# Kernel optimization log

Hardware: AMD Instinct MI355X
Metric: run time of the kernel (lower is better)

Reference implementation:

```python
import jax, jax.numpy as jnp
import numpy as np

N_NODES = 50000
N_EDGES = 800000
N_GRAPHS = 64
F_IN = 128
HEADS = 4
CH = 32
HID = HEADS * CH  # 128
N_CLASSES = 10
N_LAYERS = 3
NEG_SLOPE = 0.2


def setup_inputs() -> dict:
    key = jax.random.key(0)
    ks = jax.random.split(key, 12)
    x = jax.random.normal(ks[0], (N_NODES, F_IN), dtype=jnp.float32)
    edge_index = jax.random.randint(ks[1], (2, N_EDGES), 0, N_NODES, dtype=jnp.int64)
    batch = jnp.sort(jax.random.randint(ks[2], (N_NODES,), 0, N_GRAPHS, dtype=jnp.int64))
    s = 0.1
    Wl = jax.random.normal(ks[3], (N_LAYERS, F_IN, HID), dtype=jnp.float32) * s
    Wr = jax.random.normal(ks[4], (N_LAYERS, F_IN, HID), dtype=jnp.float32) * s
    bl = jax.random.normal(ks[5], (N_LAYERS, HID), dtype=jnp.float32) * s
    br = jax.random.normal(ks[6], (N_LAYERS, HID), dtype=jnp.float32) * s
    att = jax.random.normal(ks[7], (N_LAYERS, HEADS, CH), dtype=jnp.float32) * s
    bias = jax.random.normal(ks[8], (N_LAYERS, HID), dtype=jnp.float32) * s
    lin_w = jax.random.normal(ks[9], (HID, N_CLASSES), dtype=jnp.float32) * s
    lin_b = jax.random.normal(ks[10], (N_CLASSES,), dtype=jnp.float32) * s
    return {"x": x, "edge_index": edge_index, "batch": batch, "Wl": Wl, "Wr": Wr,
            "bl": bl, "br": br, "att": att, "bias": bias, "lin_w": lin_w, "lin_b": lin_b}


def gatv2_layer(x, Wl, Wr, bl, br, att, bias, src, dst):
    # x: [N, D_in] -> out: [N, HEADS*CH]
    n = x.shape[0]
    xl = (x @ Wl + bl).reshape(n, HEADS, CH)  # source transform
    xr = (x @ Wr + br).reshape(n, HEADS, CH)  # target transform
    # GATv2 edge scores: a^T LeakyReLU(W_l x_j + W_r x_i), per head
    e = jnp.einsum('ehc,hc->eh', jax.nn.leaky_relu(xl[src] + xr[dst], NEG_SLOPE), att)  # [E, H]
    # softmax over edges sharing the same destination node
    m = jax.ops.segment_max(e, dst, num_segments=n)
    ee = jnp.exp(e - m[dst])
    denom = jax.ops.segment_sum(ee, dst, num_segments=n)
    alpha = ee / denom[dst]  # [E, H]
    out = jax.ops.segment_sum(xl[src] * alpha[:, :, None], dst, num_segments=n)  # [N, H, C]
    return out.reshape(n, HID) + bias


def reference(x, edge_index, batch, Wl, Wr, bl, br, att, bias, lin_w, lin_b):
    n = x.shape[0]
    loop = jnp.arange(n, dtype=edge_index.dtype)
    src = jnp.concatenate([edge_index[0], loop])  # self loops (PyG default)
    dst = jnp.concatenate([edge_index[1], loop])
    h = x
    for l in range(N_LAYERS):
        h = jax.nn.elu(gatv2_layer(h, Wl[l], Wr[l], bl[l], br[l], att[l], bias[l], src, dst))
    # global mean pool over graphs
    sums = jax.ops.segment_sum(h, batch, num_segments=N_GRAPHS)
    cnt = jax.ops.segment_sum(jnp.ones((n,), h.dtype), batch, num_segments=N_GRAPHS)
    pooled = sums / jnp.maximum(cnt, 1.0)[:, None]
    logits = jax.nn.elu(pooled @ lin_w + lin_b)
    return jax.nn.log_softmax(logits, axis=1)
```

## Files before the change

### kernel.cpp

```cpp
#include <hip/hip_runtime.h>
#include <hip/hip_bf16.h>
#include <math.h>

#define N_NODES 50000
#define N_EDGES 800000
#define N_GRAPHS 64
#define HID 128
#define N_CLASSES 10
#define N_LAYERS 3
#define NEG_SLOPE 0.2f

#define NB 196
#define BCAP 5120
#define ACHUNK 4096

typedef __attribute__((ext_vector_type(8))) short short8;
typedef __attribute__((ext_vector_type(4))) float f32x4;
typedef __attribute__((ext_vector_type(2))) _Float16 h2;

extern "C" __device__ _Float16 __ocml_exp2_f16(_Float16);

__device__ inline ushort f2bf(float f) {
    uint u = __builtin_bit_cast(uint, f);
    u += 0x7fffu + ((u >> 16) & 1u);
    return (ushort)(u >> 16);
}
__device__ inline uint pk2bf(float a, float b) {
    return (uint)f2bf(a) | ((uint)f2bf(b) << 16);
}
__device__ inline h2 pkh(float a, float b) {
    return __builtin_bit_cast(h2, __builtin_amdgcn_cvt_pkrtz(a, b));
}


__global__ __launch_bounds__(256) void setup_kernel(
    const float* __restrict__ x, uint* __restrict__ xb, int n,
    const float* __restrict__ Wl, const float* __restrict__ Wr,
    uint* __restrict__ wt, int wtot,
    const int* __restrict__ ei, int E,
    int* __restrict__ bptr, uint* __restrict__ bbuf,
    int xqb, int wb) {
    __shared__ int hcnt[256];
    __shared__ int hexcl[256];
    __shared__ int lofs[256];
    __shared__ int delta[256];
    __shared__ uint stage[ACHUNK];
    int t = threadIdx.x;
    int blk = blockIdx.x;

    if (blk < xqb) {
        int j = blk * 256 + t;
        if (j < n * 16) {
            const float4* xp = (const float4*)x + (size_t)j * 2;
            float4 a = xp[0], b = xp[1];
            uint4 o;
            o.x = pk2bf(a.x, a.y); o.y = pk2bf(a.z, a.w);
            o.z = pk2bf(b.x, b.y); o.w = pk2bf(b.z, b.w);
            ((uint4*)xb)[j] = o;
        }
        return;
    }
    blk -= xqb;
    if (blk < wb) {
        int i = blk * 256 + t;
        if (i >= wtot) return;
        int kp = i & 63;
        int nn = (i >> 6) & 255;
        int l  = i >> 14;
        const float* W = (nn < 128) ? Wl : Wr;
        int c = nn & 127;
        wt[i] = pk2bf(W[l * 16384 + (2 * kp) * 128 + c],
                      W[l * 16384 + (2 * kp + 1) * 128 + c]);
        return;
    }
    blk -= wb;
    int total = E + n;
    int base = blk * ACHUNK;
    int cntblk = min(ACHUNK, total - base);
    hcnt[t] = 0; lofs[t] = 0;
    __syncthreads();

    uint v[16]; int bk[16];
#pragma unroll
    for (int j = 0; j < 16; ++j) {
        int e = base + j * 256 + t;
        bk[j] = -1;
        if (e < total) {
            int s, d;
            if (e < E) { s = ei[e]; d = ei[E + e]; }
            else       { s = e - E; d = e - E; }
            v[j] = ((uint)s << 16) | (uint)d;
            bk[j] = d >> 8;
            atomicAdd(&hcnt[bk[j]], 1);
        }
    }
    __syncthreads();
    int hv = hcnt[t];
    __shared__ int stmp[256];
    stmp[t] = hv;
    __syncthreads();
    for (int off = 1; off < 256; off <<= 1) {
        int u = (t >= off) ? stmp[t - off] : 0;
        __syncthreads();
        stmp[t] += u;
        __syncthreads();
    }
    hexcl[t] = stmp[t] - hv;
    __syncthreads();
#pragma unroll
    for (int j = 0; j < 16; ++j) {
        if (bk[j] >= 0) {
            int pos = hexcl[bk[j]] + atomicAdd(&lofs[bk[j]], 1);
            stage[pos] = v[j];
        }
    }
    __syncthreads();
    if (t < NB) {
        int c = hcnt[t];
        int gb = c ? atomicAdd(&bptr[t], c) : 0;
        delta[t] = t * BCAP + gb - hexcl[t];
    }
    __syncthreads();
    for (int idx = t; idx < cntblk; idx += 256) {
        uint val = stage[idx];
        int b = (val >> 8) & 0xff;
        int tgt = delta[b] + idx;
        if (tgt < (b + 1) * BCAP) bbuf[tgt] = val;
    }
}


__device__ __forceinline__ void gemm_body(
    const ushort* __restrict__ A, const ushort* __restrict__ Wt,
    const float* __restrict__ bl, const float* __restrict__ br,
    ushort* __restrict__ xlb, ushort* __restrict__ xrb, int n, int bid, int tid) {
    int wv = tid >> 6;
    int lane = tid & 63;
    int q = lane >> 4, m16 = lane & 15;
    int m0 = bid * 64;

    short8 bf[4][4];
#pragma unroll
    for (int nt = 0; nt < 4; ++nt) {
        const ushort* wp = Wt + (size_t)(wv * 64 + nt * 16 + m16) * 128 + q * 8;
#pragma unroll
        for (int ks = 0; ks < 4; ++ks) bf[nt][ks] = *(const short8*)(wp + ks * 32);
    }
    const ushort* ap[4];
#pragma unroll
    for (int mt = 0; mt < 4; ++mt) {
        int r = m0 + mt * 16 + m16;
        if (r > n - 1) r = n - 1;
        ap[mt] = A + (size_t)r * 128 + q * 8;
    }

    f32x4 z = {0.f, 0.f, 0.f, 0.f};
    f32x4 acc[4][4];
#pragma unroll
    for (int mt = 0; mt < 4; ++mt)
#pragma unroll
        for (int nt = 0; nt < 4; ++nt) acc[mt][nt] = z;

#pragma unroll
    for (int ks = 0; ks < 4; ++ks) {
        short8 af[4];
#pragma unroll
        for (int mt = 0; mt < 4; ++mt) af[mt] = *(const short8*)(ap[mt] + ks * 32);
#pragma unroll
        for (int mt = 0; mt < 4; ++mt)
#pragma unroll
            for (int nt = 0; nt < 4; ++nt)
                acc[mt][nt] = __builtin_amdgcn_mfma_f32_16x16x32_bf16(
                    bf[nt][ks], af[mt], acc[mt][nt], 0, 0, 0);
    }

    ushort* outp = (wv >= 2) ? xrb : xlb;
    const float* bx = (wv >= 2) ? br : bl;
    int fb = (wv & 1) * 64;
#pragma unroll
    for (int nt = 0; nt < 4; ++nt) {
        int fcol = fb + nt * 16 + q * 4;
        float4 b4 = *(const float4*)&bx[fcol];
#pragma unroll
        for (int mt = 0; mt < 4; ++mt) {
            int m = m0 + mt * 16 + m16;
            if (m < n) {
                uint2 pk;
                pk.x = __builtin_bit_cast(uint, pkh(acc[mt][nt][0] + b4.x,
                                                    acc[mt][nt][1] + b4.y));
                pk.y = __builtin_bit_cast(uint, pkh(acc[mt][nt][2] + b4.z,
                                                    acc[mt][nt][3] + b4.w));
                *(uint2*)&outp[(size_t)m * 128 + fcol] = pk;
            }
        }
    }
}

__global__ __launch_bounds__(256) void csr_gemm0_kernel(
    const int* __restrict__ bptr, const uint* __restrict__ bbuf, int n,
    int* __restrict__ row_start, int* __restrict__ ssrc,
    const ushort* __restrict__ A, const ushort* __restrict__ Wt,
    const float* __restrict__ bl, const float* __restrict__ br,
    ushort* __restrict__ xlb, ushort* __restrict__ xrb) {
    int t = threadIdx.x;
    if (blockIdx.x >= NB) {
        gemm_body(A, Wt, bl, br, xlb, xrb, n, blockIdx.x - NB, t);
        return;
    }
    int b = blockIdx.x;
    __shared__ int sb[256], h[256], hx[256], lofs[256];
    int bv = (t < NB) ? min(bptr[t], BCAP) : 0;
    sb[t] = bv;
    __syncthreads();
    for (int off = 1; off < 256; off <<= 1) {
        int u = (t >= off) ? sb[t - off] : 0;
        __syncthreads();
        sb[t] += u;
        __syncthreads();
    }
    int cnt = min(bptr[b], BCAP);
    int base = sb[b] - cnt;
    if (b == NB - 1 && t == 0) row_start[n] = sb[NB - 1];
    h[t] = 0; lofs[t] = 0;
    __syncthreads();
    const uint* bp = bbuf + (size_t)b * BCAP;
    for (int k = t; k < cnt; k += 256) atomicAdd(&h[bp[k] & 255u], 1);
    __syncthreads();
    int hv = h[t];
    hx[t] = hv;
    __syncthreads();
    for (int off = 1; off < 256; off <<= 1) {
        int u = (t >= off) ? hx[t - off] : 0;
        __syncthreads();
        hx[t] += u;
        __syncthreads();
    }
    int excl = hx[t] - hv;
    int node = (b << 8) + t;
    if (node < n) row_start[node] = base + excl;
    __syncthreads();
    h[t] = excl;
    __syncthreads();
    for (int k = t; k < cnt; k += 256) {
        uint val = bp[k];
        int dl = val & 255u;
        int pos = base + h[dl] + atomicAdd(&lofs[dl], 1);
        ssrc[pos] = (int)((val & 0xffff0000u) >> 8);
    }
}

__global__ __launch_bounds__(256) void gemm_mfma(
    const ushort* __restrict__ A, const ushort* __restrict__ Wt,
    const float* __restrict__ bl, const float* __restrict__ br,
    ushort* __restrict__ xlb, ushort* __restrict__ xrb, int n) {
    gemm_body(A, Wt, bl, br, xlb, xrb, n, blockIdx.x, threadIdx.x);
}


#define SLOTE4(u, v01, v23, v45, v67, eh)                  \
    h2 v01 = __builtin_bit_cast(h2, u.x);                  \
    h2 v23 = __builtin_bit_cast(h2, u.y);                  \
    h2 v45 = __builtin_bit_cast(h2, u.z);                  \
    h2 v67 = __builtin_bit_cast(h2, u.w);                  \
    h2 eh;                                                 \
    {                                                      \
        h2 t01 = v01 + xr01, t23 = v23 + xr23;             \
        h2 t45 = v45 + xr45, t67 = v67 + xr67;             \
        t01 = __builtin_elementwise_max(t01, t01 * K02);   \
        t23 = __builtin_elementwise_max(t23, t23 * K02);   \
        t45 = __builtin_elementwise_max(t45, t45 * K02);   \
        t67 = __builtin_elementwise_max(t67, t67 * K02);   \
        eh = EINIT + at01 * t01;                           \
        eh += at23 * t23;                                  \
        eh += at45 * t45;                                  \
        eh += at67 * t67;                                  \
    }

__device__ inline uint packpair(h2 a, h2 b) {
    h2 lo = {a.x, b.x};
    h2 hi = {a.y, b.y};
    return __builtin_bit_cast(uint, lo + hi);
}
__device__ inline uint shfl_add_h2(uint q, int m) {
    uint r = (uint)__shfl_xor((int)q, m);
    h2 s = __builtin_bit_cast(h2, q) + __builtin_bit_cast(h2, r);
    return __builtin_bit_cast(uint, s);
}

__global__ __launch_bounds__(256) void attn_kernel(
    const uint* __restrict__ xlb, const uint* __restrict__ xrb,
    const float* __restrict__ att, const float* __restrict__ bias,
    const int* __restrict__ row_start, const int* __restrict__ ssrc,
    uint* __restrict__ hout, int n) {
    int wave = threadIdx.x >> 6;
    int lane = threadIdx.x & 63;
    int g    = lane >> 4;
    int l16  = lane & 15;
    int i = blockIdx.x * 4 + wave;
    if (i >= n) return;

    const char* xlB = (const char*)xlb;
    uint lofs = (uint)l16 * 16;

    uint4 xru = *(const uint4*)((const char*)xrb + (size_t)i * 256 + lofs);
    h2 xr01 = __builtin_bit_cast(h2, xru.x);
    h2 xr23 = __builtin_bit_cast(h2, xru.y);
    h2 xr45 = __builtin_bit_cast(h2, xru.z);
    h2 xr67 = __builtin_bit_cast(h2, xru.w);
    const float L2E = 1.4426950408889634f;
    float4 atA = ((const float4*)att)[l16 * 2];
    float4 atB = ((const float4*)att)[l16 * 2 + 1];
    h2 at01 = pkh(atA.x * L2E, atA.y * L2E);
    h2 at23 = pkh(atA.z * L2E, atA.w * L2E);
    h2 at45 = pkh(atB.x * L2E, atB.y * L2E);
    h2 at67 = pkh(atB.z * L2E, atB.w * L2E);
    const h2 K02   = {(_Float16)0.2f, (_Float16)0.2f};
    const h2 EINIT = {(_Float16)-1.0f, (_Float16)-1.0f};

    int p0 = row_start[i], p1 = row_start[i + 1];

    h2 denP = {0, 0};
    h2 aA01 = {0, 0}, aA23 = {0, 0}, aA45 = {0, 0}, aA67 = {0, 0};
    h2 aB01 = {0, 0}, aB23 = {0, 0}, aB45 = {0, 0}, aB67 = {0, 0};

    int p = p0;
    for (; p + 16 <= p1; p += 16) {
        uint s0 = (uint)ssrc[p + g];
        uint s1 = (uint)ssrc[p + 4 + g];
        uint s2 = (uint)ssrc[p + 8 + g];
        uint s3 = (uint)ssrc[p + 12 + g];
        uint4 u0 = *(const uint4*)(xlB + s0 + lofs);
        uint4 u1 = *(const uint4*)(xlB + s1 + lofs);
        uint4 u2 = *(const uint4*)(xlB + s2 + lofs);
        uint4 u3 = *(const uint4*)(xlB + s3 + lofs);
        SLOTE4(u0, v001, v023, v045, v067, eh0);
        SLOTE4(u1, v101, v123, v145, v167, eh1);
        SLOTE4(u2, v201, v223, v245, v267, eh2);
        SLOTE4(u3, v301, v323, v345, v367, eh3);
        uint q01 = packpair(eh0, eh1);
        uint q23 = packpair(eh2, eh3);
        q01 = shfl_add_h2(q01, 1); q23 = shfl_add_h2(q23, 1);
        q01 = shfl_add_h2(q01, 2); q23 = shfl_add_h2(q23, 2);
        h2 e01 = __builtin_bit_cast(h2, q01);
        h2 e23 = __builtin_bit_cast(h2, q23);
        h2 w01, w23;
        w01.x = __ocml_exp2_f16(e01.x); w01.y = __ocml_exp2_f16(e01.y);
        w23.x = __ocml_exp2_f16(e23.x); w23.y = __ocml_exp2_f16(e23.y);
        denP += w01; denP += w23;
        h2 wA = {w01.x, w01.x}, wB = {w01.y, w01.y};
        h2 wC = {w23.x, w23.x}, wD = {w23.y, w23.y};
        aA01 += wA * v001; aA23 += wA * v023; aA45 += wA * v045; aA67 += wA * v067;
        aB01 += wB * v101; aB23 += wB * v123; aB45 += wB * v145; aB67 += wB * v167;
        aA01 += wC * v201; aA23 += wC * v223; aA45 += wC * v245; aA67 += wC * v267;
        aB01 += wD * v301; aB23 += wD * v323; aB45 += wD * v345; aB67 += wD * v367;
    }
    for (; p + 8 <= p1; p += 8) {
        uint s0 = (uint)ssrc[p + g];
        uint s1 = (uint)ssrc[p + 4 + g];
        uint4 u0 = *(const uint4*)(xlB + s0 + lofs);
        uint4 u1 = *(const uint4*)(xlB + s1 + lofs);
        SLOTE4(u0, v001, v023, v045, v067, eh0);
        SLOTE4(u1, v101, v123, v145, v167, eh1);
        uint q01 = packpair(eh0, eh1);
        q01 = shfl_add_h2(q01, 1);
        q01 = shfl_add_h2(q01, 2);
        h2 e01 = __builtin_bit_cast(h2, q01);
        h2 w01;
        w01.x = __ocml_exp2_f16(e01.x); w01.y = __ocml_exp2_f16(e01.y);
        denP += w01;
        h2 wA = {w01.x, w01.x}, wB = {w01.y, w01.y};
        aA01 += wA * v001; aA23 += wA * v023; aA45 += wA * v045; aA67 += wA * v067;
        aB01 += wB * v101; aB23 += wB * v123; aB45 += wB * v145; aB67 += wB * v167;
    }
    if (p < p1) {
        int lst = p1 - 1;
        int i0 = p + g, i1 = p + 4 + g;
        uint s0 = (uint)ssrc[min(i0, lst)];
        uint s1 = (uint)ssrc[min(i1, lst)];
        uint4 u0 = *(const uint4*)(xlB + s0 + lofs);
        uint4 u1 = *(const uint4*)(xlB + s1 + lofs);
        SLOTE4(u0, v001, v023, v045, v067, eh0);
        SLOTE4(u1, v101, v123, v145, v167, eh1);
        uint q01 = packpair(eh0, eh1);
        q01 = shfl_add_h2(q01, 1);
        q01 = shfl_add_h2(q01, 2);
        h2 e01 = __builtin_bit_cast(h2, q01);
        h2 w01;
        const _Float16 zh = (_Float16)0.f;
        w01.x = (i0 < p1) ? __ocml_exp2_f16(e01.x) : zh;
        w01.y = (i1 < p1) ? __ocml_exp2_f16(e01.y) : zh;
        denP += w01;
        h2 wA = {w01.x, w01.x}, wB = {w01.y, w01.y};
        aA01 += wA * v001; aA23 += wA * v023; aA45 += wA * v045; aA67 += wA * v067;
        aB01 += wB * v101; aB23 += wB * v123; aB45 += wB * v145; aB67 += wB * v167;
    }

    float den = (float)denP.x + (float)denP.y;
    float a0 = (float)(_Float16)(aA01.x + aB01.x);
    float a1 = (float)(_Float16)(aA01.y + aB01.y);
    float a2 = (float)(_Float16)(aA23.x + aB23.x);
    float a3 = (float)(_Float16)(aA23.y + aB23.y);
    float a4 = (float)(_Float16)(aA45.x + aB45.x);
    float a5 = (float)(_Float16)(aA45.y + aB45.y);
    float a6 = (float)(_Float16)(aA67.x + aB67.x);
    float a7 = (float)(_Float16)(aA67.y + aB67.y);
    den += __shfl_xor(den, 16); den += __shfl_xor(den, 32);
    a0 += __shfl_xor(a0, 16); a0 += __shfl_xor(a0, 32);
    a1 += __shfl_xor(a1, 16); a1 += __shfl_xor(a1, 32);
    a2 += __shfl_xor(a2, 16); a2 += __shfl_xor(a2, 32);
    a3 += __shfl_xor(a3, 16); a3 += __shfl_xor(a3, 32);
    a4 += __shfl_xor(a4, 16); a4 += __shfl_xor(a4, 32);
    a5 += __shfl_xor(a5, 16); a5 += __shfl_xor(a5, 32);
    a6 += __shfl_xor(a6, 16); a6 += __shfl_xor(a6, 32);
    a7 += __shfl_xor(a7, 16); a7 += __shfl_xor(a7, 32);

    if (g == 0) {
        float inv = 1.f / den;
        float4 biA = ((const float4*)bias)[l16 * 2];
        float4 biB = ((const float4*)bias)[l16 * 2 + 1];
        float o0 = a0 * inv + biA.x; o0 = o0 > 0.f ? o0 : __expf(o0) - 1.f;
        float o1 = a1 * inv + biA.y; o1 = o1 > 0.f ? o1 : __expf(o1) - 1.f;
        float o2 = a2 * inv + biA.z; o2 = o2 > 0.f ? o2 : __expf(o2) - 1.f;
        float o3 = a3 * inv + biA.w; o3 = o3 > 0.f ? o3 : __expf(o3) - 1.f;
        float o4 = a4 * inv + biB.x; o4 = o4 > 0.f ? o4 : __expf(o4) - 1.f;
        float o5 = a5 * inv + biB.y; o5 = o5 > 0.f ? o5 : __expf(o5) - 1.f;
        float o6 = a6 * inv + biB.z; o6 = o6 > 0.f ? o6 : __expf(o6) - 1.f;
        float o7 = a7 * inv + biB.w; o7 = o7 > 0.f ? o7 : __expf(o7) - 1.f;
        uint4 pk;
        pk.x = pk2bf(o0, o1);
        pk.y = pk2bf(o2, o3);
        pk.z = pk2bf(o4, o5);
        pk.w = pk2bf(o6, o7);
        *(uint4*)((char*)hout + (size_t)i * 256 + lofs) = pk;
    }
}


__device__ inline float bflo(uint v) { return __builtin_bit_cast(float, v << 16); }
__device__ inline float bfhi(uint v) { return __builtin_bit_cast(float, v & 0xffff0000u); }

__global__ __launch_bounds__(256) void pool_kernel(const uint* __restrict__ h2v,
                                                   const int* __restrict__ batch, int n,
                                                   float* __restrict__ psum) {
    int g = blockIdx.x;
    int t = threadIdx.x;
    int cp = t & 63;
    int sub = (t >> 6) | (blockIdx.y << 2);
    int b, e;
    {
        int lo = 0, hi = n;
        while (lo < hi) { int mid = (lo + hi) >> 1; if (batch[mid] < g) lo = mid + 1; else hi = mid; }
        b = lo;
        lo = 0; hi = n;
        int g1 = g + 1;
        while (lo < hi) { int mid = (lo + hi) >> 1; if (batch[mid] < g1) lo = mid + 1; else hi = mid; }
        e = lo;
    }
    float a0 = 0.f, a1 = 0.f;
    for (int i = b + sub; i < e; i += 32) {
        uint u = h2v[(size_t)i * 64 + cp];
        a0 += bflo(u); a1 += bfhi(u);
    }
    __shared__ float r0[256], r1[256];
    r0[t] = a0; r1[t] = a1;
    __syncthreads();
    if (t < 64) {
        float s0 = r0[t] + r0[t + 64] + r0[t + 128] + r0[t + 192];
        float s1 = r1[t] + r1[t + 64] + r1[t + 128] + r1[t + 192];
        atomicAdd(&psum[g * 128 + 2 * t], s0);
        atomicAdd(&psum[g * 128 + 2 * t + 1], s1);
    }
}

__global__ void final_kernel(const float* __restrict__ psum, const int* __restrict__ batch,
                             int n, const float* __restrict__ lw,
                             const float* __restrict__ lb, float* __restrict__ out) {
    int g = threadIdx.x;
    if (g >= N_GRAPHS) return;
    int b, e;
    {
        int lo = 0, hi = n;
        while (lo < hi) { int mid = (lo + hi) >> 1; if (batch[mid] < g) lo = mid + 1; else hi = mid; }
        b = lo;
        lo = 0; hi = n;
        int g1 = g + 1;
        while (lo < hi) { int mid = (lo + hi) >> 1; if (batch[mid] < g1) lo = mid + 1; else hi = mid; }
        e = lo;
    }
    float invc = 1.f / fmaxf((float)(e - b), 1.f);
    float z[N_CLASSES];
#pragma unroll
    for (int c = 0; c < N_CLASSES; ++c) z[c] = lb[c];
    for (int k = 0; k < 128; ++k) {
        float p = psum[g * 128 + k] * invc;
#pragma unroll
        for (int c = 0; c < N_CLASSES; ++c) z[c] += p * lw[k * N_CLASSES + c];
    }
    float mx = -1e30f;
#pragma unroll
    for (int c = 0; c < N_CLASSES; ++c) {
        z[c] = z[c] > 0.f ? z[c] : expf(z[c]) - 1.f;
        mx = fmaxf(mx, z[c]);
    }
    float s = 0.f;
#pragma unroll
    for (int c = 0; c < N_CLASSES; ++c) s += expf(z[c] - mx);
    float lse = mx + logf(s);
#pragma unroll
    for (int c = 0; c < N_CLASSES; ++c) out[g * N_CLASSES + c] = z[c] - lse;
}


extern "C" void kernel_launch(void* const* d_in, const int* in_sizes, int n_in,
                              void* d_out, int out_size, void* d_ws, size_t ws_size,
                              hipStream_t stream) {
    const float* x     = (const float*)d_in[0];
    const int*   ei    = (const int*)d_in[1];
    const int*   batch = (const int*)d_in[2];
    const float* Wl    = (const float*)d_in[3];
    const float* Wr    = (const float*)d_in[4];
    const float* bl    = (const float*)d_in[5];
    const float* br    = (const float*)d_in[6];
    const float* att   = (const float*)d_in[7];
    const float* bias  = (const float*)d_in[8];
    const float* lw    = (const float*)d_in[9];
    const float* lb    = (const float*)d_in[10];
    float* out = (float*)d_out;

    const int n = in_sizes[2];
    const int E = in_sizes[1] / 2;
    const int total_edges = E + n;

    char* ws = (char*)d_ws;
    size_t o = 0;
    auto alloc = [&](size_t bytes) -> void* {
        void* p = ws + o;
        o = (o + bytes + 255) & ~(size_t)255;
        return p;
    };
    int*    row_start = (int*)alloc((size_t)(n + 1) * 4);
    int*    bptr      = (int*)alloc((size_t)NB * 4);
    uint*   bbuf      = (uint*)alloc((size_t)NB * BCAP * 4);
    int*    ssrc      = (int*)alloc((size_t)total_edges * 4);
    ushort* xbf0      = (ushort*)alloc((size_t)n * HID * 2);
    ushort* xlb       = (ushort*)alloc((size_t)n * HID * 2);
    ushort* xrb       = (ushort*)alloc((size_t)n * HID * 2);
    ushort* hbA       = (ushort*)alloc((size_t)n * HID * 2);
    ushort* hbB       = (ushort*)alloc((size_t)n * HID * 2);
    uint*   wt        = (uint*)alloc((size_t)N_LAYERS * 256 * 64 * 4);
    float*  psum      = (float*)alloc((size_t)N_GRAPHS * HID * 4);

    hipMemsetAsync(bptr, 0, (size_t)NB * 4, stream);
    hipMemsetAsync(psum, 0, (size_t)N_GRAPHS * HID * 4, stream);

    int wtot = N_LAYERS * 256 * 64;
    int xqb = (n * 16 + 255) / 256;
    int wb  = (wtot + 255) / 256;
    int pb  = (total_edges + ACHUNK - 1) / ACHUNK;
    setup_kernel<<<xqb + wb + pb, 256, 0, stream>>>(
        x, (uint*)xbf0, n, Wl, Wr, wt, wtot, ei, E, bptr, bbuf, xqb, wb);

    int mblocks = (n + 63) / 64;
    int ablocks = (n + 3) / 4;

    csr_gemm0_kernel<<<NB + mblocks, 256, 0, stream>>>(
        bptr, bbuf, n, row_start, ssrc,
        xbf0, (const ushort*)wt, bl, br, xlb, xrb);

    attn_kernel<<<ablocks, 256, 0, stream>>>((const uint*)xlb, (const uint*)xrb,
                                             att, bias, row_start, ssrc, (uint*)hbA, n);
    gemm_mfma<<<mblocks, 256, 0, stream>>>(hbA, (const ushort*)(wt + (size_t)256 * 64),
                                           bl + HID, br + HID, xlb, xrb, n);
    attn_kernel<<<ablocks, 256, 0, stream>>>((const uint*)xlb, (const uint*)xrb,
                                             att + HID, bias + HID, row_start, ssrc,
                                             (uint*)hbB, n);
    gemm_mfma<<<mblocks, 256, 0, stream>>>(hbB, (const ushort*)(wt + (size_t)2 * 256 * 64),
                                           bl + 2 * HID, br + 2 * HID, xlb, xrb, n);
    attn_kernel<<<ablocks, 256, 0, stream>>>((const uint*)xlb, (const uint*)xrb,
                                             att + 2 * HID, bias + 2 * HID, row_start, ssrc,
                                             (uint*)hbA, n);

    pool_kernel<<<dim3(N_GRAPHS, 8), 256, 0, stream>>>((const uint*)hbA, batch, n, psum);
    final_kernel<<<1, 64, 0, stream>>>(psum, batch, n, lw, lb, out);
}
```

Baseline: 333.1 us.

## Map one destination node per 16-lane group in GATv2 attention kernel

The attention kernel now assigns each 16-lane quarter-wave its own destination node, so a wave handles four nodes instead of splitting one node's edges across four groups. This removes the cross-group shuffle reductions of the accumulators and the final g==0 store branch. Edge scores are reduced with DPP moves instead of shfl_xor, and the source indices for the next iteration are prefetched in software. The cost is load imbalance: every group in a wave runs for the maximum degree among its four nodes, with masked edges doing wasted gathers.

Result: faster. 322.0 us (-3.4%).

```diff
diff --git a/kernel.cpp b/kernel.cpp
--- a/kernel.cpp
+++ b/kernel.cpp
@@ -257,12 +257,12 @@
 }
 
 
-#define SLOTE4(u, v01, v23, v45, v67, eh)                  \
+#define ESCORE(u, v01, v23, v45, v67, es)                  \
     h2 v01 = __builtin_bit_cast(h2, u.x);                  \
     h2 v23 = __builtin_bit_cast(h2, u.y);                  \
     h2 v45 = __builtin_bit_cast(h2, u.z);                  \
     h2 v67 = __builtin_bit_cast(h2, u.w);                  \
-    h2 eh;                                                 \
+    _Float16 es;                                           \
     {                                                      \
         h2 t01 = v01 + xr01, t23 = v23 + xr23;             \
         h2 t45 = v45 + xr45, t67 = v67 + xr67;             \
@@ -270,19 +270,16 @@
         t23 = __builtin_elementwise_max(t23, t23 * K02);   \
         t45 = __builtin_elementwise_max(t45, t45 * K02);   \
         t67 = __builtin_elementwise_max(t67, t67 * K02);   \
-        eh = EINIT + at01 * t01;                           \
+        h2 eh = EINIT + at01 * t01;                        \
         eh += at23 * t23;                                  \
         eh += at45 * t45;                                  \
         eh += at67 * t67;                                  \
-    }
-
-__device__ inline uint packpair(h2 a, h2 b) {
-    h2 lo = {a.x, b.x};
-    h2 hi = {a.y, b.y};
-    return __builtin_bit_cast(uint, lo + hi);
-}
-__device__ inline uint shfl_add_h2(uint q, int m) {
-    uint r = (uint)__shfl_xor((int)q, m);
+        es = eh.x + eh.y;                                  \
+    }
+
+template <int CTRL>
+__device__ inline uint dpp_add_h2(uint q) {
+    uint r = (uint)__builtin_amdgcn_mov_dpp((int)q, CTRL, 0xF, 0xF, true);
     h2 s = __builtin_bit_cast(h2, q) + __builtin_bit_cast(h2, r);
     return __builtin_bit_cast(uint, s);
 }
@@ -296,8 +293,8 @@
     int lane = threadIdx.x & 63;
     int g    = lane >> 4;
     int l16  = lane & 15;
-    int i = blockIdx.x * 4 + wave;
-    if (i >= n) return;
+    int i0n  = blockIdx.x * 16 + wave * 4 + g;
+    int i    = min(i0n, n - 1);
 
     const char* xlB = (const char*)xlb;
     uint lofs = (uint)l16 * 16;
@@ -318,114 +315,81 @@
     const h2 EINIT = {(_Float16)-1.0f, (_Float16)-1.0f};
 
     int p0 = row_start[i], p1 = row_start[i + 1];
-
-    h2 denP = {0, 0};
-    h2 aA01 = {0, 0}, aA23 = {0, 0}, aA45 = {0, 0}, aA67 = {0, 0};
-    h2 aB01 = {0, 0}, aB23 = {0, 0}, aB45 = {0, 0}, aB67 = {0, 0};
-
-    int p = p0;
-    for (; p + 16 <= p1; p += 16) {
-        uint s0 = (uint)ssrc[p + g];
-        uint s1 = (uint)ssrc[p + 4 + g];
-        uint s2 = (uint)ssrc[p + 8 + g];
-        uint s3 = (uint)ssrc[p + 12 + g];
+    int d = p1 - p0;
+    int m = max(d, __shfl_xor(d, 16));
+    m = max(m, __shfl_xor(m, 32));
+    int iters = (m + 3) >> 2;
+    int lst = p1 - 1;
+
+    _Float16 denA = (_Float16)0.f, denB = (_Float16)0.f;
+    h2 aE01 = {0, 0}, aE23 = {0, 0}, aE45 = {0, 0}, aE67 = {0, 0};
+    h2 aO01 = {0, 0}, aO23 = {0, 0}, aO45 = {0, 0}, aO67 = {0, 0};
+
+    int idx = p0;
+    uint s0 = (uint)ssrc[idx];
+    uint s1 = (uint)ssrc[min(idx + 1, lst)];
+    uint s2 = (uint)ssrc[min(idx + 2, lst)];
+    uint s3 = (uint)ssrc[min(idx + 3, lst)];
+
+    for (int it = 0; it < iters; ++it) {
         uint4 u0 = *(const uint4*)(xlB + s0 + lofs);
         uint4 u1 = *(const uint4*)(xlB + s1 + lofs);
         uint4 u2 = *(const uint4*)(xlB + s2 + lofs);
         uint4 u3 = *(const uint4*)(xlB + s3 + lofs);
-        SLOTE4(u0, v001, v023, v045, v067, eh0);
-        SLOTE4(u1, v101, v123, v145, v167, eh1);
-        SLOTE4(u2, v201, v223, v245, v267, eh2);
-        SLOTE4(u3, v301, v323, v345, v367, eh3);
-        uint q01 = packpair(eh0, eh1);
-        uint q23 = packpair(eh2, eh3);
-        q01 = shfl_add_h2(q01, 1); q23 = shfl_add_h2(q23, 1);
-        q01 = shfl_add_h2(q01, 2); q23 = shfl_add_h2(q23, 2);
+        bool b0 = idx     < p1;
+        bool b1 = idx + 1 < p1;
+        bool b2 = idx + 2 < p1;
+        bool b3 = idx + 3 < p1;
+        int nidx = idx + 4;
+        uint ns0 = (uint)ssrc[min(nidx,     lst)];
+        uint ns1 = (uint)ssrc[min(nidx + 1, lst)];
+        uint ns2 = (uint)ssrc[min(nidx + 2, lst)];
+        uint ns3 = (uint)ssrc[min(nidx + 3, lst)];
+        ESCORE(u0, v001, v023, v045, v067, es0);
+        ESCORE(u1, v101, v123, v145, v167, es1);
+        ESCORE(u2, v201, v223, v245, v267, es2);
+        ESCORE(u3, v301, v323, v345, v367, es3);
+        h2 q01h; q01h.x = es0; q01h.y = es1;
+        h2 q23h; q23h.x = es2; q23h.y = es3;
+        uint q01 = __builtin_bit_cast(uint, q01h);
+        uint q23 = __builtin_bit_cast(uint, q23h);
+        q01 = dpp_add_h2<0xB1>(q01);
+        q23 = dpp_add_h2<0xB1>(q23);
+        q01 = dpp_add_h2<0x4E>(q01);
+        q23 = dpp_add_h2<0x4E>(q23);
         h2 e01 = __builtin_bit_cast(h2, q01);
         h2 e23 = __builtin_bit_cast(h2, q23);
-        h2 w01, w23;
-        w01.x = __ocml_exp2_f16(e01.x); w01.y = __ocml_exp2_f16(e01.y);
-        w23.x = __ocml_exp2_f16(e23.x); w23.y = __ocml_exp2_f16(e23.y);
-        denP += w01; denP += w23;
-        h2 wA = {w01.x, w01.x}, wB = {w01.y, w01.y};
-        h2 wC = {w23.x, w23.x}, wD = {w23.y, w23.y};
-        aA01 += wA * v001; aA23 += wA * v023; aA45 += wA * v045; aA67 += wA * v067;
-        aB01 += wB * v101; aB23 += wB * v123; aB45 += wB * v145; aB67 += wB * v167;
-        aA01 += wC * v201; aA23 += wC * v223; aA45 += wC * v245; aA67 += wC * v267;
-        aB01 += wD * v301; aB23 += wD * v323; aB45 += wD * v345; aB67 += wD * v367;
-    }
-    for (; p + 8 <= p1; p += 8) {
-        uint s0 = (uint)ssrc[p + g];
-        uint s1 = (uint)ssrc[p + 4 + g];
-        uint4 u0 = *(const uint4*)(xlB + s0 + lofs);
-        uint4 u1 = *(const uint4*)(xlB + s1 + lofs);
-        SLOTE4(u0, v001, v023, v045, v067, eh0);
-        SLOTE4(u1, v101, v123, v145, v167, eh1);
-        uint q01 = packpair(eh0, eh1);
-        q01 = shfl_add_h2(q01, 1);
-        q01 = shfl_add_h2(q01, 2);
-        h2 e01 = __builtin_bit_cast(h2, q01);
-        h2 w01;
-        w01.x = __ocml_exp2_f16(e01.x); w01.y = __ocml_exp2_f16(e01.y);
-        denP += w01;
-        h2 wA = {w01.x, w01.x}, wB = {w01.y, w01.y};
-        aA01 += wA * v001; aA23 += wA * v023; aA45 += wA * v045; aA67 += wA * v067;
-        aB01 += wB * v101; aB23 += wB * v123; aB45 += wB * v145; aB67 += wB * v167;
-    }
-    if (p < p1) {
-        int lst = p1 - 1;
-        int i0 = p + g, i1 = p + 4 + g;
-        uint s0 = (uint)ssrc[min(i0, lst)];
-        uint s1 = (uint)ssrc[min(i1, lst)];
-        uint4 u0 = *(const uint4*)(xlB + s0 + lofs);
-        uint4 u1 = *(const uint4*)(xlB + s1 + lofs);
-        SLOTE4(u0, v001, v023, v045, v067, eh0);
-        SLOTE4(u1, v101, v123, v145, v167, eh1);
-        uint q01 = packpair(eh0, eh1);
-        q01 = shfl_add_h2(q01, 1);
-        q01 = shfl_add_h2(q01, 2);
-        h2 e01 = __builtin_bit_cast(h2, q01);
-        h2 w01;
         const _Float16 zh = (_Float16)0.f;
-        w01.x = (i0 < p1) ? __ocml_exp2_f16(e01.x) : zh;
-        w01.y = (i1 < p1) ? __ocml_exp2_f16(e01.y) : zh;
-        denP += w01;
-        h2 wA = {w01.x, w01.x}, wB = {w01.y, w01.y};
-        aA01 += wA * v001; aA23 += wA * v023; aA45 += wA * v045; aA67 += wA * v067;
-        aB01 += wB * v101; aB23 += wB * v123; aB45 += wB * v145; aB67 += wB * v167;
-    }
-
-    float den = (float)denP.x + (float)denP.y;
-    float a0 = (float)(_Float16)(aA01.x + aB01.x);
-    float a1 = (float)(_Float16)(aA01.y + aB01.y);
-    float a2 = (float)(_Float16)(aA23.x + aB23.x);
-    float a3 = (float)(_Float16)(aA23.y + aB23.y);
-    float a4 = (float)(_Float16)(aA45.x + aB45.x);
-    float a5 = (float)(_Float16)(aA45.y + aB45.y);
-    float a6 = (float)(_Float16)(aA67.x + aB67.x);
-    float a7 = (float)(_Float16)(aA67.y + aB67.y);
-    den += __shfl_xor(den, 16); den += __shfl_xor(den, 32);
-    a0 += __shfl_xor(a0, 16); a0 += __shfl_xor(a0, 32);
-    a1 += __shfl_xor(a1, 16); a1 += __shfl_xor(a1, 32);
-    a2 += __shfl_xor(a2, 16); a2 += __shfl_xor(a2, 32);
-    a3 += __shfl_xor(a3, 16); a3 += __shfl_xor(a3, 32);
-    a4 += __shfl_xor(a4, 16); a4 += __shfl_xor(a4, 32);
-    a5 += __shfl_xor(a5, 16); a5 += __shfl_xor(a5, 32);
-    a6 += __shfl_xor(a6, 16); a6 += __shfl_xor(a6, 32);
-    a7 += __shfl_xor(a7, 16); a7 += __shfl_xor(a7, 32);
-
-    if (g == 0) {
-        float inv = 1.f / den;
-        float4 biA = ((const float4*)bias)[l16 * 2];
-        float4 biB = ((const float4*)bias)[l16 * 2 + 1];
-        float o0 = a0 * inv + biA.x; o0 = o0 > 0.f ? o0 : __expf(o0) - 1.f;
-        float o1 = a1 * inv + biA.y; o1 = o1 > 0.f ? o1 : __expf(o1) - 1.f;
-        float o2 = a2 * inv + biA.z; o2 = o2 > 0.f ? o2 : __expf(o2) - 1.f;
-        float o3 = a3 * inv + biA.w; o3 = o3 > 0.f ? o3 : __expf(o3) - 1.f;
-        float o4 = a4 * inv + biB.x; o4 = o4 > 0.f ? o4 : __expf(o4) - 1.f;
-        float o5 = a5 * inv + biB.y; o5 = o5 > 0.f ? o5 : __expf(o5) - 1.f;
-        float o6 = a6 * inv + biB.z; o6 = o6 > 0.f ? o6 : __expf(o6) - 1.f;
-        float o7 = a7 * inv + biB.w; o7 = o7 > 0.f ? o7 : __expf(o7) - 1.f;
+        _Float16 w0 = b0 ? __ocml_exp2_f16(e01.x) : zh;
+        _Float16 w1 = b1 ? __ocml_exp2_f16(e01.y) : zh;
+        _Float16 w2 = b2 ? __ocml_exp2_f16(e23.x) : zh;
+        _Float16 w3 = b3 ? __ocml_exp2_f16(e23.y) : zh;
+        denA += w0; denB += w1; denA += w2; denB += w3;
+        h2 wA = {w0, w0}, wB = {w1, w1}, wC = {w2, w2}, wD = {w3, w3};
+        aE01 += wA * v001; aE23 += wA * v023; aE45 += wA * v045; aE67 += wA * v067;
+        aO01 += wB * v101; aO23 += wB * v123; aO45 += wB * v145; aO67 += wB * v167;
+        aE01 += wC * v201; aE23 += wC * v223; aE45 += wC * v245; aE67 += wC * v267;
+        aO01 += wD * v301; aO23 += wD * v323; aO45 += wD * v345; aO67 += wD * v367;
+        idx = nidx; s0 = ns0; s1 = ns1; s2 = ns2; s3 = ns3;
+    }
+
+    float den = (float)denA + (float)denB;
+    float inv = 1.f / den;
+    h2 a01 = aE01 + aO01;
+    h2 a23 = aE23 + aO23;
+    h2 a45 = aE45 + aO45;
+    h2 a67 = aE67 + aO67;
+    float4 biA = ((const float4*)bias)[l16 * 2];
+    float4 biB = ((const float4*)bias)[l16 * 2 + 1];
+    float o0 = (float)a01.x * inv + biA.x; o0 = o0 > 0.f ? o0 : __expf(o0) - 1.f;
+    float o1 = (float)a01.y * inv + biA.y; o1 = o1 > 0.f ? o1 : __expf(o1) - 1.f;
+    float o2 = (float)a23.x * inv + biA.z; o2 = o2 > 0.f ? o2 : __expf(o2) - 1.f;
+    float o3 = (float)a23.y * inv + biA.w; o3 = o3 > 0.f ? o3 : __expf(o3) - 1.f;
+    float o4 = (float)a45.x * inv + biB.x; o4 = o4 > 0.f ? o4 : __expf(o4) - 1.f;
+    float o5 = (float)a45.y * inv + biB.y; o5 = o5 > 0.f ? o5 : __expf(o5) - 1.f;
+    float o6 = (float)a67.x * inv + biB.z; o6 = o6 > 0.f ? o6 : __expf(o6) - 1.f;
+    float o7 = (float)a67.y * inv + biB.w; o7 = o7 > 0.f ? o7 : __expf(o7) - 1.f;
+    if (i0n < n) {
         uint4 pk;
         pk.x = pk2bf(o0, o1);
         pk.y = pk2bf(o2, o3);
@@ -561,7 +525,7 @@
         x, (uint*)xbf0, n, Wl, Wr, wt, wtot, ei, E, bptr, bbuf, xqb, wb);
 
     int mblocks = (n + 63) / 64;
-    int ablocks = (n + 3) / 4;
+    int ablocks = (n + 15) / 16;
 
     csr_gemm0_kernel<<<NB + mblocks, 256, 0, stream>>>(
         bptr, bbuf, n, row_start, ssrc,
```
